# Kernel optimization log

Hardware: AMD Instinct MI355X
Metric: run time of the kernel (lower is better)

Reference implementation:

```python
import jax, jax.numpy as jnp
import numpy as np

EMBED_DIM = 2048
N_HEADS = 16
D_HEAD = EMBED_DIM // N_HEADS


def setup_inputs() -> dict:
    key = jax.random.key(0)
    kx, kq, kk, kv = jax.random.split(key, 4)
    B, N, D = 4, 2048, EMBED_DIM
    x = jax.random.normal(kx, (B, N, D), dtype=jnp.float32)
    Wq = jax.random.normal(kq, (D, D), dtype=jnp.float32) * 0.02
    Wk = jax.random.normal(kk, (D, D), dtype=jnp.float32) * 0.02
    Wv = jax.random.normal(kv, (D, D), dtype=jnp.float32) * 0.02
    return {"x": x, "Wq": Wq, "Wk": Wk, "Wv": Wv}


def reference(x, Wq, Wk, Wv):
    # x: [B, N, D]; weights applied as x @ W (matching torch.matmul in source)
    B, N, D = x.shape
    H, d = N_HEADS, D_HEAD
    # [B, N, D] -> [B, H, N, d]
    Q = (x @ Wq).reshape(B, N, H, d).transpose(0, 2, 1, 3)
    K = (x @ Wk).reshape(B, N, H, d).transpose(0, 2, 1, 3)
    V = (x @ Wv).reshape(B, N, H, d).transpose(0, 2, 1, 3)
    scale = 1.0 / jnp.sqrt(jnp.asarray(d, dtype=x.dtype))
    # non-causal SDPA (torch default: no mask, scale = 1/sqrt(d_head))
    scores = jnp.einsum('bhqd,bhkd->bhqk', Q, K) * scale  # [B,H,N,N]
    attn = jax.nn.softmax(scores, axis=-1)
    out = jnp.einsum('bhqk,bhkd->bhqd', attn, V)  # [B,H,N,d]
    return out
```

## Files before the change

### kernel.cpp

```cpp
#include <hip/hip_runtime.h>
#include <hip/hip_bf16.h>

#define B 4
#define N 2048
#define D 2048
#define H 16
#define DH 128
#define NT 32

typedef unsigned short u16;
typedef __attribute__((ext_vector_type(8))) short short8;
typedef __attribute__((ext_vector_type(4))) float floatx4;

__device__ __forceinline__ u16 f2b(float f) {
    union { __hip_bfloat16 h; u16 u; } cv;
    cv.h = __float2bfloat16(f);
    return cv.u;
}

__device__ __forceinline__ floatx4 mfma16(short8 a, short8 b, floatx4 c) {
    return __builtin_amdgcn_mfma_f32_16x16x32_bf16(a, b, c, 0, 0, 0);
}

#if __has_builtin(__builtin_amdgcn_exp2f)
#define EXP2(x) __builtin_amdgcn_exp2f(x)
#else
#define EXP2(x) exp2f(x)
#endif

__device__ __forceinline__ void async16(const void* g, void* l) {
    __builtin_amdgcn_global_load_lds(
        (const __attribute__((address_space(1))) unsigned int*)g,
        (__attribute__((address_space(3))) unsigned int*)l, 16, 0, 0);
}

__global__ __launch_bounds__(256) void cvt_x(const float* __restrict__ x,
                                             u16* __restrict__ xb) {
    size_t i = ((size_t)blockIdx.x * 256 + threadIdx.x) * 8;
    float4 v0 = *(const float4*)&x[i];
    float4 v1 = *(const float4*)&x[i + 4];
    union { u16 u[8]; uint4 s; } pk;
    pk.u[0] = f2b(v0.x); pk.u[1] = f2b(v0.y); pk.u[2] = f2b(v0.z); pk.u[3] = f2b(v0.w);
    pk.u[4] = f2b(v1.x); pk.u[5] = f2b(v1.y); pk.u[6] = f2b(v1.z); pk.u[7] = f2b(v1.w);
    *(uint4*)&xb[i] = pk.s;
}

__global__ __launch_bounds__(256) void cvt_w_t(const float* __restrict__ Wq,
                                               const float* __restrict__ Wk,
                                               const float* __restrict__ Wv,
                                               u16* __restrict__ wt) {
    __shared__ float tile[64][65];
    const int z = blockIdx.z;
    const float* W = (z == 0) ? Wq : (z == 1) ? Wk : Wv;
    const float scl = (z == 0) ? 0.12751743342f : 1.0f;
    const int k0 = blockIdx.x * 64, n0 = blockIdx.y * 64;
    const int tr = threadIdx.x >> 4, tc = threadIdx.x & 15;
#pragma unroll
    for (int i = 0; i < 4; i++) {
        int kk = tr + 16 * i;
        float4 vv = *(const float4*)&W[(size_t)(k0 + kk) * D + n0 + tc * 4];
        tile[kk][tc * 4 + 0] = vv.x; tile[kk][tc * 4 + 1] = vv.y;
        tile[kk][tc * 4 + 2] = vv.z; tile[kk][tc * 4 + 3] = vv.w;
    }
    __syncthreads();
#pragma unroll
    for (int i = 0; i < 4; i++) {
        int nn = tr + 16 * i;
        union { u16 u[4]; ushort4 s; } pk;
#pragma unroll
        for (int j = 0; j < 4; j++) pk.u[j] = f2b(tile[tc * 4 + j][nn] * scl);
        *(ushort4*)&wt[(size_t)z * D * D + (size_t)(n0 + nn) * D + k0 + tc * 4] = pk.s;
    }
}

#define KT 32
#define SGB __builtin_amdgcn_sched_group_barrier
__global__ __launch_bounds__(512, 2) void qkv_gemm(const u16* __restrict__ xb,
                                                   const u16* __restrict__ wt,
                                                   u16* __restrict__ qo,
                                                   u16* __restrict__ ko,
                                                   u16* __restrict__ vo) {
    __shared__ u16 lds[2][2][2][128 * 64];

    const int bid = blockIdx.x;
    const int c = bid & 7, i = bid >> 3;
    const int i6 = (i * 43) >> 8;
    const int tm = ((c >> 2) << 4) + i6;
    const int tn = (c & 3) * 6 + (i - 6 * i6);

    const int t = threadIdx.x, lane = t & 63, w = t >> 6;
    const int wr = w >> 2, wc = w & 3;
    const int q4 = lane >> 4, lr = lane & 15;

    const int m0 = tm * 256;
    const int n0 = tn * 256;

    unsigned aoff[2][2], boff[2][2];
#pragma unroll
    for (int ii = 0; ii < 2; ii++) {
        const int off = ii * 8192 + w * 1024 + lane * 16;
        const int row = off >> 7;
        const int s = (off >> 4) & 7;
        const int col = ((s ^ (row & 7))) * 8;
#pragma unroll
        for (int h = 0; h < 2; h++) {
            aoff[h][ii] = (unsigned)((m0 + h * 128 + row) * D + col);
            boff[h][ii] = (unsigned)((n0 + h * 128 + row) * D + col);
        }
    }

    const unsigned cb0 = (unsigned)(((0 * 4 + q4) ^ (lr & 7)) * 16);
    const unsigned cb1 = (unsigned)(((1 * 4 + q4) ^ (lr & 7)) * 16);
    unsigned aB0 = (unsigned)(wr * 16384 + lr * 128) + cb0;
    unsigned aB1 = (unsigned)(wr * 16384 + lr * 128) + cb1;
    unsigned bB0 = (unsigned)(32768 + (wc >> 1) * 16384 + (wc & 1) * 8192 + lr * 128) + cb0;
    unsigned bB1 = (unsigned)(32768 + (wc >> 1) * 16384 + (wc & 1) * 8192 + lr * 128) + cb1;

#define STAGE_A(buf, h, j) {                                                        \
    async16(xb + aoff[h][0] + (unsigned)(j) * 64, (char*)&lds[buf][0][h][0] + w * 1024);        \
    async16(xb + aoff[h][1] + (unsigned)(j) * 64, (char*)&lds[buf][0][h][0] + 8192 + w * 1024); }
#define STAGE_B(buf, h, j) {                                                        \
    async16(wt + boff[h][0] + (unsigned)(j) * 64, (char*)&lds[buf][1][h][0] + w * 1024);        \
    async16(wt + boff[h][1] + (unsigned)(j) * 64, (char*)&lds[buf][1][h][0] + 8192 + w * 1024); }
#define BAR() __builtin_amdgcn_s_barrier()
#define DSR(base, imm) (*(const short8*)((const char*)&lds[0][0][0][0] + (base) + (imm)))

    floatx4 acc[8][4];
#pragma unroll
    for (int x = 0; x < 8; x++)
#pragma unroll
        for (int j = 0; j < 4; j++) acc[x][j] = (floatx4){0.f, 0.f, 0.f, 0.f};

    STAGE_A(0, 0, 0); STAGE_A(0, 1, 0);
    STAGE_B(0, 0, 0); STAGE_B(0, 1, 0);
    STAGE_A(1, 0, 1); STAGE_A(1, 1, 1);
    asm volatile("s_waitcnt vmcnt(4)" ::: "memory");
    BAR();

    for (int g = 0; g < KT; g++) {
        const int cur = g & 1, nxt = cur ^ 1;

        if (g + 1 < KT) { STAGE_B(nxt, 0, g + 1); STAGE_B(nxt, 1, g + 1); }

        short8 a0k0[4], a0k1[4], a1k0[4], a1k1[4];
        short8 b0k0[2], b0k1[2], b1k0[2], b1k1[2];

        b0k0[0] = DSR(bB0, 0);    b0k0[1] = DSR(bB0, 2048);
#pragma unroll
        for (int mf = 0; mf < 4; mf++) a0k0[mf] = DSR(aB0, mf * 2048);
        b0k1[0] = DSR(bB1, 0);    b0k1[1] = DSR(bB1, 2048);
#pragma unroll
        for (int mf = 0; mf < 4; mf++) a0k1[mf] = DSR(aB1, mf * 2048);

#pragma unroll
        for (int nf = 0; nf < 2; nf++)
#pragma unroll
            for (int mf = 0; mf < 4; mf++)
                acc[mf][nf] = mfma16(a0k0[mf], b0k0[nf], acc[mf][nf]);

#pragma unroll
        for (int mf = 0; mf < 4; mf++) a1k0[mf] = DSR(aB0, 8192 + mf * 2048);
        b1k0[0] = DSR(bB0, 4096); b1k0[1] = DSR(bB0, 6144);

#pragma unroll
        for (int nf = 0; nf < 2; nf++)
#pragma unroll
            for (int mf = 0; mf < 4; mf++)
                acc[mf][nf] = mfma16(a0k1[mf], b0k1[nf], acc[mf][nf]);

#pragma unroll
        for (int mf = 0; mf < 4; mf++) a1k1[mf] = DSR(aB1, 8192 + mf * 2048);
        b1k1[0] = DSR(bB1, 4096); b1k1[1] = DSR(bB1, 6144);

#pragma unroll
        for (int nf = 0; nf < 2; nf++)
#pragma unroll
            for (int mf = 0; mf < 4; mf++)
                acc[4 + mf][nf] = mfma16(a1k0[mf], b0k0[nf], acc[4 + mf][nf]);

#pragma unroll
        for (int nf = 0; nf < 2; nf++)
#pragma unroll
            for (int mf = 0; mf < 4; mf++)
                acc[4 + mf][nf] = mfma16(a1k1[mf], b0k1[nf], acc[4 + mf][nf]);

        SGB(0x100, 12, 0);
        SGB(0x008,  8, 0);
        SGB(0x100,  6, 0);
        SGB(0x008,  8, 0);
        SGB(0x100,  6, 0);
        SGB(0x008,  8, 0);
        SGB(0x008,  8, 0);

        BAR();

        if (g + 2 < KT) { STAGE_A(cur, 0, g + 2); STAGE_A(cur, 1, g + 2); }

        __builtin_amdgcn_s_setprio(1);
#pragma unroll
        for (int nf = 0; nf < 2; nf++)
#pragma unroll
            for (int mf = 0; mf < 4; mf++)
                acc[4 + mf][2 + nf] = mfma16(a1k0[mf], b1k0[nf], acc[4 + mf][2 + nf]);
#pragma unroll
        for (int nf = 0; nf < 2; nf++)
#pragma unroll
            for (int mf = 0; mf < 4; mf++)
                acc[4 + mf][2 + nf] = mfma16(a1k1[mf], b1k1[nf], acc[4 + mf][2 + nf]);
#pragma unroll
        for (int nf = 0; nf < 2; nf++)
#pragma unroll
            for (int mf = 0; mf < 4; mf++) {
                acc[mf][2 + nf] = mfma16(a0k0[mf], b1k0[nf], acc[mf][2 + nf]);
                acc[mf][2 + nf] = mfma16(a0k1[mf], b1k1[nf], acc[mf][2 + nf]);
            }
        __builtin_amdgcn_s_setprio(0);

        if (g == KT - 2) { asm volatile("s_waitcnt vmcnt(0)" ::: "memory"); }
        else if (g < KT - 2) { asm volatile("s_waitcnt vmcnt(4)" ::: "memory"); }
        if (g + 1 < KT) BAR();

        aB0 ^= 65536u; aB1 ^= 65536u; bB0 ^= 65536u; bB1 ^= 65536u;
    }

    const int z = tn >> 3;
    u16* dst = (z == 0) ? qo : (z == 1) ? ko : vo;
    const int c2b = (tn & 7) * 256 + wc * 64;
    const int grb = tm * 256 + wr * 128;
#pragma unroll
    for (int mf = 0; mf < 8; mf++)
#pragma unroll
        for (int nf = 0; nf < 4; nf++)
#pragma unroll
            for (int r = 0; r < 4; r++) {
                int gr = grb + mf * 16 + q4 * 4 + r;
                int c2 = c2b + nf * 16 + lr;
                int b_ = gr >> 11, n_ = gr & (N - 1);
                int head = c2 >> 7, dcol = c2 & 127;
                dst[((size_t)(b_ * H + head) * N + n_) * DH + dcol] = f2b(acc[mf][nf][r]);
            }
#undef STAGE_A
#undef STAGE_B
#undef BAR
#undef DSR
}

__global__ __launch_bounds__(256) void transpose_v(const u16* __restrict__ v,
                                                   u16* __restrict__ vt) {
    __shared__ u16 tile[64][72];
    const int bh = blockIdx.z;
    const int n0 = blockIdx.x * 64, d0 = blockIdx.y * 64;
    const int t = threadIdx.x;
#pragma unroll
    for (int i = 0; i < 2; i++) {
        int gid = t + 256 * i;
        int nl = gid >> 3, g = gid & 7;
        *(uint4*)&tile[nl][g * 8] =
            *(const uint4*)&v[((size_t)bh * N + n0 + nl) * DH + d0 + g * 8];
    }
    __syncthreads();
#pragma unroll
    for (int i = 0; i < 2; i++) {
        int gid = t + 256 * i;
        int dl = gid >> 3, gn = gid & 7;
        union { u16 u[8]; uint4 s; } pk;
#pragma unroll
        for (int j = 0; j < 8; j++) {
            int kp = gn * 8 + j;
            int src = 32 * (kp >> 5) + 16 * (kp & 1) + ((kp >> 1) & 15);
            pk.u[j] = tile[src][dl];
        }
        *(uint4*)&vt[((size_t)bh * DH + d0 + dl) * N + n0 + gn * 8] = pk.s;
    }
}

#define FMAX2 17.312340491f
__global__ __launch_bounds__(256, 2) void attn_kernel(const u16* __restrict__ q,
                                                      const u16* __restrict__ k,
                                                      const u16* __restrict__ vt,
                                                      float* __restrict__ out) {
    __shared__ u16 Ks[2][64][128];
    __shared__ u16 Vts[2][128][64];
    __shared__ u16 Ps[128][64];

    const int beta = blockIdx.x;
    const int bh = (beta & 7) + 8 * (beta >> 7);
    const int qt = (beta >> 3) & 15;
    const int t = threadIdx.x;
    const int w = t >> 6, lane = t & 63;
    const int half = lane >> 4, lr = lane & 15;
    const int a = w & 1, b = w >> 1;

    const size_t qbase = ((size_t)bh * N + (size_t)qt * 128) * DH;
    short8 af[4][4];
#pragma unroll
    for (int rt = 0; rt < 4; rt++)
#pragma unroll
        for (int ks = 0; ks < 4; ks++)
            af[rt][ks] = *(const short8*)&q[qbase + (size_t)(64 * b + 16 * rt + lr) * DH
                                            + ks * 32 + half * 8];

    float lrow[4][4];
    floatx4 o[4][4];
#pragma unroll
    for (int rt = 0; rt < 4; rt++)
#pragma unroll
        for (int r = 0; r < 4; r++) lrow[rt][r] = 0.f;
#pragma unroll
    for (int rt = 0; rt < 4; rt++)
#pragma unroll
        for (int ct = 0; ct < 4; ct++) o[rt][ct] = (floatx4){0.f, 0.f, 0.f, 0.f};

    const size_t kbase = (size_t)bh * N * DH;
    const size_t vtbase = (size_t)bh * DH * N;
    const u16* kp[4];
    const u16* vp[4];
#pragma unroll
    for (int c = 0; c < 4; c++) {
        int grp = 4 * w + c;
        int krow = 4 * grp + (lane >> 4);
        int kg = (lane & 15) ^ (krow & 15);
        kp[c] = &k[kbase + (size_t)krow * DH + kg * 8];
        int vrow = 8 * grp + (lane >> 3);
        int vg = (lane & 7) ^ (vrow & 7);
        vp[c] = &vt[vtbase + (size_t)vrow * N + vg * 8];
    }

#pragma unroll
    for (int c = 0; c < 4; c++) {
        async16(kp[c], (char*)&Ks[0][0][0] + (4 * w + c) * 1024);
        async16(vp[c], (char*)&Vts[0][0][0] + (4 * w + c) * 1024);
    }

    for (int kt = 0; kt < NT; kt++) {
        const int cur = kt & 1;
        __syncthreads();

        floatx4 sf[4][2];
#pragma unroll
        for (int ct = 0; ct < 2; ct++) {
            short8 bf[4];
#pragma unroll
            for (int ks = 0; ks < 4; ks++) {
                int gs = (4 * ks + half) ^ lr;
                bf[ks] = *(const short8*)&Ks[cur][32 * a + 16 * ct + lr][gs * 8];
            }
#pragma unroll
            for (int rt = 0; rt < 4; rt++) {
                floatx4 s = (floatx4){0.f, 0.f, 0.f, 0.f};
#pragma unroll
                for (int ks = 0; ks < 4; ks++) s = mfma16(af[rt][ks], bf[ks], s);
                sf[rt][ct] = s;
            }
        }

#pragma unroll
        for (int rt = 0; rt < 4; rt++)
#pragma unroll
            for (int r = 0; r < 4; r++) {
                int row = 64 * b + 16 * rt + 4 * half + r;
                float p0 = EXP2(sf[rt][0][r] - FMAX2);
                float p1 = EXP2(sf[rt][1][r] - FMAX2);
                lrow[rt][r] += p0 + p1;
                unsigned int pw = (unsigned int)f2b(p0) | ((unsigned int)f2b(p1) << 16);
                int u = (16 * a + lr) ^ ((row & 7) << 2);
                *(unsigned int*)&Ps[row][u * 2] = pw;
            }

        __syncthreads();

        if (kt + 1 < NT) {
            const int nb = cur ^ 1;
#pragma unroll
            for (int c = 0; c < 4; c++) {
                async16(kp[c] + (size_t)(kt + 1) * 64 * DH,
                        (char*)&Ks[nb][0][0] + (4 * w + c) * 1024);
                async16(vp[c] + (size_t)(kt + 1) * 64,
                        (char*)&Vts[nb][0][0] + (4 * w + c) * 1024);
            }
        }

#pragma unroll
        for (int ks = 0; ks < 2; ks++) {
            short8 a2[4];
#pragma unroll
            for (int rt = 0; rt < 4; rt++) {
                int g = (4 * ks + half) ^ (lr & 7);
                a2[rt] = *(const short8*)&Ps[64 * b + 16 * rt + lr][g * 8];
            }
#pragma unroll
            for (int ct = 0; ct < 4; ct++) {
                int dd = 64 * a + 16 * ct + lr;
                int gv = (4 * ks + half) ^ (lr & 7);
                short8 bv = *(const short8*)&Vts[cur][dd][gv * 8];
#pragma unroll
                for (int rt = 0; rt < 4; rt++)
                    o[rt][ct] = mfma16(a2[rt], bv, o[rt][ct]);
            }
        }
    }

    __syncthreads();
    float* Ls = (float*)&Ps[0][0];
#pragma unroll
    for (int rt = 0; rt < 4; rt++)
#pragma unroll
        for (int r = 0; r < 4; r++) {
            float s = lrow[rt][r];
            s += __shfl_xor(s, 1);
            s += __shfl_xor(s, 2);
            s += __shfl_xor(s, 4);
            s += __shfl_xor(s, 8);
            if (lr == 0) Ls[a * 128 + (64 * b + 16 * rt + 4 * half + r)] = s;
        }
    __syncthreads();
    const size_t obase = ((size_t)bh * N + (size_t)qt * 128) * DH;
#pragma unroll
    for (int rt = 0; rt < 4; rt++)
#pragma unroll
        for (int r = 0; r < 4; r++) {
            int row = 64 * b + 16 * rt + 4 * half + r;
            float inv = 1.f / (Ls[row] + Ls[128 + row]);
#pragma unroll
            for (int ct = 0; ct < 4; ct++)
                out[obase + (size_t)row * DH + 64 * a + 16 * ct + lr] = o[rt][ct][r] * inv;
        }
}

extern "C" void kernel_launch(void* const* d_in, const int* in_sizes, int n_in,
                              void* d_out, int out_size, void* d_ws, size_t ws_size,
                              hipStream_t stream) {
    const float* x  = (const float*)d_in[0];
    const float* Wq = (const float*)d_in[1];
    const float* Wk = (const float*)d_in[2];
    const float* Wv = (const float*)d_in[3];
    float* out = (float*)d_out;
    char* ws = (char*)d_ws;

    u16* xb = (u16*)(ws);
    u16* wt = (u16*)(ws + 33554432);
    u16* qb = (u16*)(ws + 58720256);
    u16* kb = (u16*)(ws + 92274688);
    u16* vb = (u16*)(ws + 125829120);
    u16* vtb = (u16*)(ws);

    cvt_x<<<dim3(8192), dim3(256), 0, stream>>>(x, xb);
    cvt_w_t<<<dim3(32, 32, 3), dim3(256), 0, stream>>>(Wq, Wk, Wv, wt);
    qkv_gemm<<<dim3(768), dim3(512), 0, stream>>>(xb, wt, qb, kb, vb);
    transpose_v<<<dim3(32, 2, 64), dim3(256), 0, stream>>>(vb, vtb);
    attn_kernel<<<dim3(1024), dim3(256), 0, stream>>>(qb, kb, vtb, out);
}
```

Before: 484.0 us.

## Triple-buffer A tiles in LDS and drop mid-iteration barrier in QKV GEMM

```diff
diff --git a/kernel.cpp b/kernel.cpp
--- a/kernel.cpp
+++ b/kernel.cpp
@@ -80,7 +80,7 @@
                                                    u16* __restrict__ qo,
                                                    u16* __restrict__ ko,
                                                    u16* __restrict__ vo) {
-    __shared__ u16 lds[2][2][2][128 * 64];
+    __shared__ u16 lds[81920];
 
     const int bid = blockIdx.x;
     const int c = bid & 7, i = bid >> 3;
@@ -111,19 +111,23 @@
 
     const unsigned cb0 = (unsigned)(((0 * 4 + q4) ^ (lr & 7)) * 16);
     const unsigned cb1 = (unsigned)(((1 * 4 + q4) ^ (lr & 7)) * 16);
-    unsigned aB0 = (unsigned)(wr * 16384 + lr * 128) + cb0;
-    unsigned aB1 = (unsigned)(wr * 16384 + lr * 128) + cb1;
-    unsigned bB0 = (unsigned)(32768 + (wc >> 1) * 16384 + (wc & 1) * 8192 + lr * 128) + cb0;
-    unsigned bB1 = (unsigned)(32768 + (wc >> 1) * 16384 + (wc & 1) * 8192 + lr * 128) + cb1;
-
-#define STAGE_A(buf, h, j) {                                                        \
-    async16(xb + aoff[h][0] + (unsigned)(j) * 64, (char*)&lds[buf][0][h][0] + w * 1024);        \
-    async16(xb + aoff[h][1] + (unsigned)(j) * 64, (char*)&lds[buf][0][h][0] + 8192 + w * 1024); }
-#define STAGE_B(buf, h, j) {                                                        \
-    async16(wt + boff[h][0] + (unsigned)(j) * 64, (char*)&lds[buf][1][h][0] + w * 1024);        \
-    async16(wt + boff[h][1] + (unsigned)(j) * 64, (char*)&lds[buf][1][h][0] + 8192 + w * 1024); }
+    const unsigned aC0 = (unsigned)(wr * 16384 + lr * 128) + cb0;
+    const unsigned aC1 = (unsigned)(wr * 16384 + lr * 128) + cb1;
+    const unsigned bC0 = (unsigned)((wc >> 1) * 16384 + (wc & 1) * 8192 + lr * 128) + cb0;
+    const unsigned bC1 = (unsigned)((wc >> 1) * 16384 + (wc & 1) * 8192 + lr * 128) + cb1;
+
+#define STAGE_A(bufoff, h, j) {                                                           \
+    async16(xb + aoff[h][0] + (unsigned)(j) * 64,                                         \
+            (char*)lds + (bufoff) + (h) * 16384 + w * 1024);                              \
+    async16(xb + aoff[h][1] + (unsigned)(j) * 64,                                         \
+            (char*)lds + (bufoff) + (h) * 16384 + 8192 + w * 1024); }
+#define STAGE_B(bufoff, h, j) {                                                           \
+    async16(wt + boff[h][0] + (unsigned)(j) * 64,                                         \
+            (char*)lds + (bufoff) + (h) * 16384 + w * 1024);                              \
+    async16(wt + boff[h][1] + (unsigned)(j) * 64,                                         \
+            (char*)lds + (bufoff) + (h) * 16384 + 8192 + w * 1024); }
 #define BAR() __builtin_amdgcn_s_barrier()
-#define DSR(base, imm) (*(const short8*)((const char*)&lds[0][0][0][0] + (base) + (imm)))
+#define DSR(off) (*(const short8*)((const char*)lds + (off)))
 
     floatx4 acc[8][4];
 #pragma unroll
@@ -131,96 +135,102 @@
 #pragma unroll
         for (int j = 0; j < 4; j++) acc[x][j] = (floatx4){0.f, 0.f, 0.f, 0.f};
 
-    STAGE_A(0, 0, 0); STAGE_A(0, 1, 0);
-    STAGE_B(0, 0, 0); STAGE_B(0, 1, 0);
-    STAGE_A(1, 0, 1); STAGE_A(1, 1, 1);
+    STAGE_A(0u, 0, 0); STAGE_A(0u, 1, 0);
+    STAGE_B(98304u, 0, 0); STAGE_B(98304u, 1, 0);
+    STAGE_A(32768u, 0, 1); STAGE_A(32768u, 1, 1);
     asm volatile("s_waitcnt vmcnt(4)" ::: "memory");
     BAR();
 
+    unsigned aOffR = 0u;
+    unsigned aOffW = 65536u;
+
     for (int g = 0; g < KT; g++) {
-        const int cur = g & 1, nxt = cur ^ 1;
-
-        if (g + 1 < KT) { STAGE_B(nxt, 0, g + 1); STAGE_B(nxt, 1, g + 1); }
+        const unsigned bR = 98304u + (unsigned)((g & 1) << 15);
+        const unsigned bW = 98304u + (unsigned)(((g + 1) & 1) << 15);
+
+        if (g + 1 < KT) { STAGE_B(bW, 0, g + 1); STAGE_B(bW, 1, g + 1); }
+        if (g + 2 < KT) { STAGE_A(aOffW, 0, g + 2); STAGE_A(aOffW, 1, g + 2); }
+        __builtin_amdgcn_sched_barrier(0);
+
+        const unsigned aB0 = aOffR + aC0, aB1 = aOffR + aC1;
+        const unsigned bB0 = bR + bC0, bB1 = bR + bC1;
 
         short8 a0k0[4], a0k1[4], a1k0[4], a1k1[4];
         short8 b0k0[2], b0k1[2], b1k0[2], b1k1[2];
 
-        b0k0[0] = DSR(bB0, 0);    b0k0[1] = DSR(bB0, 2048);
-#pragma unroll
-        for (int mf = 0; mf < 4; mf++) a0k0[mf] = DSR(aB0, mf * 2048);
-        b0k1[0] = DSR(bB1, 0);    b0k1[1] = DSR(bB1, 2048);
-#pragma unroll
-        for (int mf = 0; mf < 4; mf++) a0k1[mf] = DSR(aB1, mf * 2048);
-
+        b0k0[0] = DSR(bB0);        b0k0[1] = DSR(bB0 + 2048);
+#pragma unroll
+        for (int mf = 0; mf < 4; mf++) a0k0[mf] = DSR(aB0 + mf * 2048);
+#pragma unroll
+        for (int mf = 0; mf < 4; mf++) a1k0[mf] = DSR(aB0 + 8192 + mf * 2048);
 #pragma unroll
         for (int nf = 0; nf < 2; nf++)
 #pragma unroll
             for (int mf = 0; mf < 4; mf++)
                 acc[mf][nf] = mfma16(a0k0[mf], b0k0[nf], acc[mf][nf]);
-
-#pragma unroll
-        for (int mf = 0; mf < 4; mf++) a1k0[mf] = DSR(aB0, 8192 + mf * 2048);
-        b1k0[0] = DSR(bB0, 4096); b1k0[1] = DSR(bB0, 6144);
-
+        b1k0[0] = DSR(bB0 + 4096); b1k0[1] = DSR(bB0 + 6144);
+#pragma unroll
+        for (int nf = 0; nf < 2; nf++)
+#pragma unroll
+            for (int mf = 0; mf < 4; mf++)
+                acc[4 + mf][nf] = mfma16(a1k0[mf], b0k0[nf], acc[4 + mf][nf]);
+        b0k1[0] = DSR(bB1);        b0k1[1] = DSR(bB1 + 2048);
+#pragma unroll
+        for (int mf = 0; mf < 4; mf++) a0k1[mf] = DSR(aB1 + mf * 2048);
+#pragma unroll
+        for (int nf = 0; nf < 2; nf++)
+#pragma unroll
+            for (int mf = 0; mf < 4; mf++)
+                acc[4 + mf][2 + nf] = mfma16(a1k0[mf], b1k0[nf], acc[4 + mf][2 + nf]);
+#pragma unroll
+        for (int mf = 0; mf < 4; mf++) a1k1[mf] = DSR(aB1 + 8192 + mf * 2048);
+#pragma unroll
+        for (int nf = 0; nf < 2; nf++)
+#pragma unroll
+            for (int mf = 0; mf < 4; mf++)
+                acc[mf][2 + nf] = mfma16(a0k0[mf], b1k0[nf], acc[mf][2 + nf]);
+        b1k1[0] = DSR(bB1 + 4096); b1k1[1] = DSR(bB1 + 6144);
 #pragma unroll
         for (int nf = 0; nf < 2; nf++)
 #pragma unroll
             for (int mf = 0; mf < 4; mf++)
                 acc[mf][nf] = mfma16(a0k1[mf], b0k1[nf], acc[mf][nf]);
-
-#pragma unroll
-        for (int mf = 0; mf < 4; mf++) a1k1[mf] = DSR(aB1, 8192 + mf * 2048);
-        b1k1[0] = DSR(bB1, 4096); b1k1[1] = DSR(bB1, 6144);
-
-#pragma unroll
-        for (int nf = 0; nf < 2; nf++)
-#pragma unroll
-            for (int mf = 0; mf < 4; mf++)
-                acc[4 + mf][nf] = mfma16(a1k0[mf], b0k0[nf], acc[4 + mf][nf]);
-
 #pragma unroll
         for (int nf = 0; nf < 2; nf++)
 #pragma unroll
             for (int mf = 0; mf < 4; mf++)
                 acc[4 + mf][nf] = mfma16(a1k1[mf], b0k1[nf], acc[4 + mf][nf]);
-
-        SGB(0x100, 12, 0);
+#pragma unroll
+        for (int nf = 0; nf < 2; nf++)
+#pragma unroll
+            for (int mf = 0; mf < 4; mf++)
+                acc[4 + mf][2 + nf] = mfma16(a1k1[mf], b1k1[nf], acc[4 + mf][2 + nf]);
+#pragma unroll
+        for (int nf = 0; nf < 2; nf++)
+#pragma unroll
+            for (int mf = 0; mf < 4; mf++)
+                acc[mf][2 + nf] = mfma16(a0k1[mf], b1k1[nf], acc[mf][2 + nf]);
+
+        SGB(0x100, 10, 0);
+        SGB(0x008,  8, 0);
+        SGB(0x100,  2, 0);
         SGB(0x008,  8, 0);
         SGB(0x100,  6, 0);
         SGB(0x008,  8, 0);
-        SGB(0x100,  6, 0);
-        SGB(0x008,  8, 0);
-        SGB(0x008,  8, 0);
-
-        BAR();
-
-        if (g + 2 < KT) { STAGE_A(cur, 0, g + 2); STAGE_A(cur, 1, g + 2); }
-
-        __builtin_amdgcn_s_setprio(1);
-#pragma unroll
-        for (int nf = 0; nf < 2; nf++)
-#pragma unroll
-            for (int mf = 0; mf < 4; mf++)
-                acc[4 + mf][2 + nf] = mfma16(a1k0[mf], b1k0[nf], acc[4 + mf][2 + nf]);
-#pragma unroll
-        for (int nf = 0; nf < 2; nf++)
-#pragma unroll
-            for (int mf = 0; mf < 4; mf++)
-                acc[4 + mf][2 + nf] = mfma16(a1k1[mf], b1k1[nf], acc[4 + mf][2 + nf]);
-#pragma unroll
-        for (int nf = 0; nf < 2; nf++)
-#pragma unroll
-            for (int mf = 0; mf < 4; mf++) {
-                acc[mf][2 + nf] = mfma16(a0k0[mf], b1k0[nf], acc[mf][2 + nf]);
-                acc[mf][2 + nf] = mfma16(a0k1[mf], b1k1[nf], acc[mf][2 + nf]);
-            }
-        __builtin_amdgcn_s_setprio(0);
+        SGB(0x100,  4, 0);
+        SGB(0x008,  8, 0);
+        SGB(0x100,  2, 0);
+        SGB(0x008,  8, 0);
+        SGB(0x008,  8, 0);
+        SGB(0x008,  8, 0);
+        SGB(0x008,  8, 0);
 
         if (g == KT - 2) { asm volatile("s_waitcnt vmcnt(0)" ::: "memory"); }
         else if (g < KT - 2) { asm volatile("s_waitcnt vmcnt(4)" ::: "memory"); }
         if (g + 1 < KT) BAR();
 
-        aB0 ^= 65536u; aB1 ^= 65536u; bB0 ^= 65536u; bB1 ^= 65536u;
+        aOffR = (aOffR == 65536u) ? 0u : aOffR + 32768u;
+        aOffW = (aOffW == 65536u) ? 0u : aOffW + 32768u;
     }
 
     const int z = tn >> 3;
```

Result: faster. 463.4 us (-4.2%).
